# Kernel tuning notes

Measured on AMD Instinct MI355X. Metric: run time of the kernel, lower is better.

Reference implementation:

```python
import jax, jax.numpy as jnp
import numpy as np

PZ = 16          # partition_size
ITERS = 3        # soft_skel iterations
ADP_SMOOTH = 1e-08
A = 0.5
B = 0.5
THRESHOLD = 0.8


def _blockify(x, pz):
    # x: (N, C, Z, X, Y) -> (N*nz*nx*ny, C, pz, pz, pz), loop order N,z,x,y
    N, C, Z, X, Y = x.shape
    nz, nx, ny = Z // pz, X // pz, Y // pz
    x = x.reshape(N, C, nz, pz, nx, pz, ny, pz)
    x = x.transpose(0, 2, 4, 6, 1, 3, 5, 7)
    return x.reshape(N * nz * nx * ny, C, pz, pz, pz)


def _maxpool3d(x, win, pad):
    # torch max_pool pads with -inf
    return jax.lax.reduce_window(
        x, -jnp.inf, jax.lax.max,
        (1, 1) + win, (1, 1, 1, 1, 1),
        ((0, 0), (0, 0), (pad[0], pad[0]), (pad[1], pad[1]), (pad[2], pad[2])))


def _minpool3d(x, win, pad):
    # -maxpool(-x) == minpool with +inf padding
    return jax.lax.reduce_window(
        x, jnp.inf, jax.lax.min,
        (1, 1) + win, (1, 1, 1, 1, 1),
        ((0, 0), (0, 0), (pad[0], pad[0]), (pad[1], pad[1]), (pad[2], pad[2])))


def _soft_erode(img):
    p1 = _minpool3d(img, (3, 1, 1), (1, 0, 0))
    p2 = _minpool3d(img, (1, 3, 1), (0, 1, 0))
    p3 = _minpool3d(img, (1, 1, 3), (0, 0, 1))
    return jnp.minimum(jnp.minimum(p1, p2), p3)


def _soft_dilate(img):
    return _maxpool3d(img, (3, 3, 3), (1, 1, 1))


def _soft_skel(img, iters):
    img1 = _soft_dilate(_soft_erode(img))
    skel = jax.nn.relu(img - img1)
    for _ in range(iters):
        img = _soft_erode(img)
        img1 = _soft_dilate(_soft_erode(img))
        delta = jax.nn.relu(img - img1)
        skel = skel + jax.nn.relu(delta - skel * delta)
    return skel


def _laplacian_bdr(x):
    # 3x3x3 kernel: all -1 with center 26; per-block conv, zero padding 1
    k = -jnp.ones((27,), dtype=x.dtype).at[13].set(26.0).reshape(1, 1, 3, 3, 3)
    b = jax.lax.conv_general_dilated(
        x, k, window_strides=(1, 1, 1), padding=[(1, 1)] * 3,
        dimension_numbers=('NCDHW', 'OIDHW', 'NCDHW'))
    # clamp(min=0) then threshold at 0.1 -> binary map (zero gradient, as in torch)
    return (b > 0.1).astype(x.dtype)


def _per_channel_dice(p, g, eps=1e-6):
    C = p.shape[1]
    pf = jnp.moveaxis(p, 1, 0).reshape(C, -1)
    gf = jnp.moveaxis(g, 1, 0).reshape(C, -1)
    intersect = jnp.sum(pf * gf, axis=-1)
    denom = jnp.sum(pf * pf, axis=-1) + jnp.sum(gf * gf, axis=-1)
    return 2.0 * intersect / jnp.maximum(denom, eps)


def _tversky_terms(p_blk, g_blk):
    # blocks: (M, C, pz, pz, pz) -> per-block adaptive Tversky loss sum
    M = p_blk.shape[0]
    pf = p_blk.reshape(M, -1)
    gf = g_blk.reshape(M, -1)
    tp = jnp.sum(gf * pf, axis=1)
    fn = jnp.sum(gf * (1.0 - pf), axis=1)
    fp = jnp.sum((1.0 - gf) * pf, axis=1)
    alpha = A + B * ((fp + ADP_SMOOTH) / (fp + fn + ADP_SMOOTH))
    beta = A + B * ((fn + ADP_SMOOTH) / (fp + fn + ADP_SMOOTH))
    return jnp.sum(1.0 - (tp + ADP_SMOOTH) / (tp + alpha * fp + beta * fn + ADP_SMOOTH))


def _forward(pred, groundtruth, w1, w2):
    dice_coeff = jnp.mean(_per_channel_dice(pred, groundtruth))
    dice_loss = 1.0 - jnp.mean(_per_channel_dice(pred, groundtruth))

    p_blk = _blockify(pred, PZ)          # (M, 1, pz, pz, pz)
    g_blk = _blockify(groundtruth, PZ)
    M = p_blk.shape[0]

    pre_bdr = _laplacian_bdr(p_blk)
    gt_bdr = _laplacian_bdr(g_blk)
    pre_cl = _soft_skel(p_blk, ITERS)
    gt_cl = _soft_skel(g_blk, ITERS)

    loss_bdr = _tversky_terms(pre_bdr, gt_bdr)
    loss_cl = _tversky_terms(pre_cl, gt_cl)

    w1s, w2s = w1[0], w2[0]
    edge_loss = (w1s ** -2 * loss_bdr + w2s ** -2 * loss_cl) / (2.0 * M) \
        + jnp.log(1.0 + jnp.abs(w1s) * jnp.abs(w2s))

    return jnp.where(dice_coeff < THRESHOLD, dice_loss, dice_loss + edge_loss)


def setup_inputs() -> dict:
    key = jax.random.key(0)
    k1, k2 = jax.random.split(key)
    shape = (2, 1, 192, 192, 192)
    gt = (jax.random.uniform(k1, shape, dtype=jnp.float32) > 0.7).astype(jnp.float32)
    # pred close to gt so dice_coeff > threshold and the adaptive branch runs
    pred = jnp.clip(gt * 0.9 + 0.05 + 0.02 * jax.random.normal(k2, shape, dtype=jnp.float32), 0.0, 1.0)
    return {
        'pred': pred,
        'groundtruth': gt,
        'w1': jnp.ones((1,), dtype=jnp.float32),
        'w2': jnp.ones((1,), dtype=jnp.float32),
    }


def reference(pred, groundtruth, w1, w2):
    return _forward(pred, groundtruth, w1, w2)
```

## Files before the change

### kernel.cpp

```cpp
#include <hip/hip_runtime.h>
#include <cmath>

#define NBLK 3456

#define DPP_SHR1 0x111
#define DPP_SHL1 0x101

template<int CTRL>
__device__ __forceinline__ float dpp_keep_f(float v) {
  return __int_as_float(__builtin_amdgcn_update_dpp(
      __float_as_int(v), __float_as_int(v), CTRL, 0xF, 0xF, false));
}
template<int CTRL>
__device__ __forceinline__ float dpp_zero_f(float v) {
  return __int_as_float(__builtin_amdgcn_update_dpp(
      0, __float_as_int(v), CTRL, 0xF, 0xF, true));
}
template<int CTRL>
__device__ __forceinline__ unsigned dpp_keep_u(unsigned v) {
  return (unsigned)__builtin_amdgcn_update_dpp((int)v, (int)v, CTRL, 0xF, 0xF, false);
}
template<int CTRL>
__device__ __forceinline__ unsigned dpp_zero_u(unsigned v) {
  return (unsigned)__builtin_amdgcn_update_dpp(0, (int)v, CTRL, 0xF, 0xF, true);
}

#define COL_IDX(c, xx) (((c)*18 + (xx) + 1)*16 + y)

__global__ __launch_bounds__(256)
void fused_blocks(const float* __restrict__ pred, const float* __restrict__ gtp,
                  float* __restrict__ ws)
{
  __shared__ float4 buf[1152];
  unsigned* m_ex = (unsigned*)buf;
  float*    red  = ((float*)buf) + 512;

  const int tid = threadIdx.x;
  const int x = tid >> 4;
  const int y = tid & 15;

  const int b  = blockIdx.x;
  const int n  = b / 1728;
  const int r  = b - n * 1728;
  const int bz = r / 144;
  const int r2 = r - bz * 144;
  const int bx = r2 / 12;
  const int by = r2 - bx * 12;

  const size_t base = (size_t)(n * 192 + bz * 16) * 36864
                    + (size_t)(bx * 16 + x) * 192 + (size_t)(by * 16 + y);

  const float INF = __builtin_inff();

  auto write_pads = [&](float pv) {
    if (tid < 128) {
      const int c  = tid >> 5;
      const int xi = ((tid >> 4) & 1) ? 17 : 0;
      const int yy = tid & 15;
      buf[(c * 18 + xi) * 16 + yy] = make_float4(pv, pv, pv, pv);
    }
  };

  float p[16];
  #pragma unroll
  for (int z = 0; z < 16; ++z) p[z] = pred[base + (size_t)z * 36864];

  unsigned gm = 0u;
  float sp2 = 0.f, spg = 0.f;
  #pragma unroll
  for (int z = 0; z < 16; ++z) {
    float gz = gtp[base + (size_t)z * 36864];
    sp2 = fmaf(p[z], p[z], sp2);
    spg = fmaf(p[z], gz, spg);
    if (gz > 0.5f) gm |= (1u << z);
  }

  float szy[16];
  {
    float sy[16];
    #pragma unroll
    for (int z = 0; z < 16; ++z) {
      float v = p[z];
      sy[z] = v + dpp_zero_f<DPP_SHR1>(v) + dpp_zero_f<DPP_SHL1>(v);
    }
    #pragma unroll
    for (int z = 0; z < 16; ++z) {
      float s = sy[z];
      if (z > 0)  s += sy[z-1];
      if (z < 15) s += sy[z+1];
      szy[z] = s;
    }
  }
  #pragma unroll
  for (int c = 0; c < 4; ++c)
    buf[COL_IDX(c, x)] = make_float4(szy[4*c], szy[4*c+1], szy[4*c+2], szy[4*c+3]);
  write_pads(0.f);
  __syncthreads();

  unsigned pm_bdr = 0u;
  #pragma unroll
  for (int c = 0; c < 4; ++c) {
    float4 a4 = buf[COL_IDX(c, x - 1)];
    float4 b4 = buf[COL_IDX(c, x + 1)];
    float sm[4] = {a4.x + b4.x, a4.y + b4.y, a4.z + b4.z, a4.w + b4.w};
    #pragma unroll
    for (int j = 0; j < 4; ++j) {
      const int z = 4*c + j;
      float bb = fmaf(27.f, p[z], -(szy[z] + sm[j]));
      if (bb > 0.1f) pm_bdr |= (1u << z);
    }
  }
  __syncthreads();

  #pragma unroll
  for (int c = 0; c < 4; ++c)
    buf[COL_IDX(c, x)] = make_float4(p[4*c], p[4*c+1], p[4*c+2], p[4*c+3]);
  write_pads(INF);
  __syncthreads();

  float cur[16], skl[16];
  #pragma unroll
  for (int z = 0; z < 16; ++z) { cur[z] = p[z]; skl[z] = 0.f; }

  for (int k = 0; k < 4; ++k) {
    float xm[16], xp[16];
    #pragma unroll
    for (int c = 0; c < 4; ++c) {
      float4 a4 = buf[COL_IDX(c, x - 1)];
      float4 b4 = buf[COL_IDX(c, x + 1)];
      xm[4*c] = a4.x; xm[4*c+1] = a4.y; xm[4*c+2] = a4.z; xm[4*c+3] = a4.w;
      xp[4*c] = b4.x; xp[4*c+1] = b4.y; xp[4*c+2] = b4.z; xp[4*c+3] = b4.w;
    }
    float en[16];
    #pragma unroll
    for (int z = 0; z < 16; ++z) {
      float v = cur[z];
      float m = fminf(v, fminf(dpp_keep_f<DPP_SHR1>(v), dpp_keep_f<DPP_SHL1>(v)));
      if (z > 0)  m = fminf(m, cur[z-1]);
      if (z < 15) m = fminf(m, cur[z+1]);
      en[z] = fminf(m, fminf(xm[z], xp[z]));
    }
    float ty[16], tz[16];
    #pragma unroll
    for (int z = 0; z < 16; ++z) {
      float v = en[z];
      ty[z] = fmaxf(v, fmaxf(dpp_keep_f<DPP_SHR1>(v), dpp_keep_f<DPP_SHL1>(v)));
    }
    #pragma unroll
    for (int z = 0; z < 16; ++z) {
      float m = ty[z];
      if (z > 0)  m = fmaxf(m, ty[z-1]);
      if (z < 15) m = fmaxf(m, ty[z+1]);
      tz[z] = m;
    }
    __syncthreads();
    #pragma unroll
    for (int c = 0; c < 4; ++c)
      buf[COL_IDX(c, x)] = make_float4(tz[4*c], tz[4*c+1], tz[4*c+2], tz[4*c+3]);
    write_pads(-INF);
    __syncthreads();
    #pragma unroll
    for (int c = 0; c < 4; ++c) {
      float4 a4 = buf[COL_IDX(c, x - 1)];
      float4 b4 = buf[COL_IDX(c, x + 1)];
      float dm[4] = {fmaxf(a4.x, b4.x), fmaxf(a4.y, b4.y),
                     fmaxf(a4.z, b4.z), fmaxf(a4.w, b4.w)};
      #pragma unroll
      for (int j = 0; j < 4; ++j) {
        const int z = 4*c + j;
        float D = fmaxf(tz[z], dm[j]);
        float delta = fmaxf(cur[z] - D, 0.f);
        skl[z] += fmaxf(fmaf(-skl[z], delta, delta), 0.f);
        cur[z] = en[z];
      }
    }
    if (k < 3) {
      __syncthreads();
      #pragma unroll
      for (int c = 0; c < 4; ++c)
        buf[COL_IDX(c, x)] = make_float4(en[4*c], en[4*c+1], en[4*c+2], en[4*c+3]);
      write_pads(INF);
      __syncthreads();
    }
  }
  __syncthreads();

  unsigned ly  = gm & dpp_zero_u<DPP_SHR1>(gm) & dpp_zero_u<DPP_SHL1>(gm);
  unsigned lzy = ly & (ly >> 1) & ((ly << 1) & 0xFFFFu);
  m_ex[(x + 1) * 16 + y] = lzy;
  if (tid < 32) m_ex[((tid >> 4) ? 17 : 0) * 16 + (tid & 15)] = 0u;
  __syncthreads();
  unsigned gm_bdr = gm & ~(m_ex[x * 16 + y] & lzy & m_ex[(x + 2) * 16 + y]);

  unsigned curm = gm, sklm = 0u;
  for (int k = 0; k < 4; ++k) {
    __syncthreads();
    m_ex[(x + 1) * 16 + y] = curm;
    if (tid < 32) m_ex[((tid >> 4) ? 17 : 0) * 16 + (tid & 15)] = 0xFFFFu;
    __syncthreads();
    unsigned em = curm
        & dpp_keep_u<DPP_SHR1>(curm) & dpp_keep_u<DPP_SHL1>(curm)
        & ((curm >> 1) | 0x8000u) & ((curm << 1) | 1u)
        & m_ex[x * 16 + y] & m_ex[(x + 2) * 16 + y];
    em &= 0xFFFFu;
    unsigned dy  = em | dpp_keep_u<DPP_SHR1>(em) | dpp_keep_u<DPP_SHL1>(em);
    unsigned dzy = (dy | (dy >> 1) | (dy << 1)) & 0xFFFFu;
    __syncthreads();
    m_ex[(x + 1) * 16 + y] = dzy;
    if (tid < 32) m_ex[((tid >> 4) ? 17 : 0) * 16 + (tid & 15)] = 0u;
    __syncthreads();
    unsigned D = m_ex[x * 16 + y] | dzy | m_ex[(x + 2) * 16 + y];
    sklm |= curm & ~D;
    curm = em;
  }

  float vals[9];
  {
    float tcl = 0.f, scl = 0.f;
    #pragma unroll
    for (int z = 0; z < 16; ++z) {
      scl += skl[z];
      tcl += ((sklm >> z) & 1u) ? skl[z] : 0.f;
    }
    vals[0] = tcl;
    vals[1] = scl;
    vals[2] = (float)__popc(sklm);
    vals[3] = (float)__popc(pm_bdr & gm_bdr);
    vals[4] = (float)__popc(pm_bdr);
    vals[5] = (float)__popc(gm_bdr);
    vals[6] = spg;
    vals[7] = sp2;
    vals[8] = (float)__popc(gm);
  }
  #pragma unroll
  for (int j = 0; j < 9; ++j) {
    float v = vals[j];
    #pragma unroll
    for (int off = 32; off; off >>= 1) v += __shfl_xor(v, off);
    vals[j] = v;
  }
  if ((tid & 63) == 0) {
    #pragma unroll
    for (int j = 0; j < 9; ++j) red[(tid >> 6) * 9 + j] = vals[j];
  }
  __syncthreads();
  if (tid == 0) {
    float t[9];
    #pragma unroll
    for (int j = 0; j < 9; ++j) t[j] = red[j] + red[9 + j] + red[18 + j] + red[27 + j];
    const float s = 1e-8f;
    float tp = t[3], fp = t[4] - t[3], fn = t[5] - t[3];
    float den = fp + fn + s;
    float alpha = 0.5f + 0.5f * ((fp + s) / den);
    float beta  = 0.5f + 0.5f * ((fn + s) / den);
    float lb = 1.f - (tp + s) / (tp + alpha * fp + beta * fn + s);
    float tpc = t[0], fpc = t[1] - t[0], fnc = t[2] - t[0];
    float denc = fpc + fnc + s;
    float alphac = 0.5f + 0.5f * ((fpc + s) / denc);
    float betac  = 0.5f + 0.5f * ((fnc + s) / denc);
    float lc = 1.f - (tpc + s) / (tpc + alphac * fpc + betac * fnc + s);
    float* o = ws + (size_t)b * 8;
    o[0] = lb; o[1] = lc; o[2] = t[6]; o[3] = t[7]; o[4] = t[8];
  }
}

__global__ __launch_bounds__(256)
void finalize_kernel(const float* __restrict__ ws, const float* __restrict__ w1p,
                     const float* __restrict__ w2p, float* __restrict__ out)
{
  __shared__ double red2[20];
  double a[5] = {0.0, 0.0, 0.0, 0.0, 0.0};
  for (int i = threadIdx.x; i < NBLK; i += 256) {
    const float* o = ws + (size_t)i * 8;
    a[0] += (double)o[0];
    a[1] += (double)o[1];
    a[2] += (double)o[2];
    a[3] += (double)o[3];
    a[4] += (double)o[4];
  }
  #pragma unroll
  for (int j = 0; j < 5; ++j) {
    double v = a[j];
    #pragma unroll
    for (int off = 32; off; off >>= 1) v += __shfl_xor(v, off);
    if ((threadIdx.x & 63) == 0) red2[(threadIdx.x >> 6) * 5 + j] = v;
  }
  __syncthreads();
  if (threadIdx.x == 0) {
    double t[5];
    #pragma unroll
    for (int j = 0; j < 5; ++j) t[j] = red2[j] + red2[5 + j] + red2[10 + j] + red2[15 + j];
    double denom = t[3] + t[4];
    if (denom < 1e-6) denom = 1e-6;
    double dice = 2.0 * t[2] / denom;
    double dl = 1.0 - dice;
    double w1 = (double)w1p[0], w2 = (double)w2p[0];
    double edge = (t[0] / (w1 * w1) + t[1] / (w2 * w2)) / (2.0 * (double)NBLK)
                + log(1.0 + fabs(w1) * fabs(w2));
    out[0] = (float)((dice < 0.8) ? dl : (dl + edge));
  }
}

extern "C" void kernel_launch(void* const* d_in, const int* in_sizes, int n_in,
                              void* d_out, int out_size, void* d_ws, size_t ws_size,
                              hipStream_t stream)
{
  const float* pred = (const float*)d_in[0];
  const float* gtp  = (const float*)d_in[1];
  const float* w1   = (const float*)d_in[2];
  const float* w2   = (const float*)d_in[3];
  float* ws = (float*)d_ws;

  fused_blocks<<<NBLK, 256, 0, stream>>>(pred, gtp, ws);
  finalize_kernel<<<1, 256, 0, stream>>>(ws, w1, w2, (float*)d_out);
}
```

Baseline: 181.0 us.

## Split each block's z-column across two threads and double-buffer shared memory

Each 16^3 block is now processed by 512 threads, with two threads per (x,y) column each owning 8 z-slices. Z-boundary neighbours are exchanged with cross-lane shuffles. Separate erode and dilate shared buffers, plus two bitmask buffers, remove several barriers per iteration and let the tz stencil be folded into the shared read. This targets per-thread register pressure and serial latency, at the cost of extra shuffles, larger shared memory per block and redundant bitmask work in the duplicated half.

```diff
diff --git a/kernel.cpp b/kernel.cpp
--- a/kernel.cpp
+++ b/kernel.cpp
@@ -25,19 +25,22 @@
   return (unsigned)__builtin_amdgcn_update_dpp(0, (int)v, CTRL, 0xF, 0xF, true);
 }
 
-#define COL_IDX(c, xx) (((c)*18 + (xx) + 1)*16 + y)
-
-__global__ __launch_bounds__(256)
+#define COL_IDX(cg, xx) (((cg)*18 + (xx) + 1)*16 + y)
+
+__global__ __launch_bounds__(512)
 void fused_blocks(const float* __restrict__ pred, const float* __restrict__ gtp,
                   float* __restrict__ ws)
 {
-  __shared__ float4 buf[1152];
-  unsigned* m_ex = (unsigned*)buf;
-  float*    red  = ((float*)buf) + 512;
+  __shared__ float4   bufE[1152];
+  __shared__ float4   bufT[1152];
+  __shared__ unsigned mA[288];
+  __shared__ unsigned mB[288];
+  float* red = (float*)mB;
 
   const int tid = threadIdx.x;
-  const int x = tid >> 4;
-  const int y = tid & 15;
+  const int y  = tid & 15;
+  const int zh = (tid >> 4) & 1;
+  const int x  = tid >> 5;
 
   const int b  = blockIdx.x;
   const int n  = b / 1728;
@@ -47,190 +50,193 @@
   const int bx = r2 / 12;
   const int by = r2 - bx * 12;
 
-  const size_t base = (size_t)(n * 192 + bz * 16) * 36864
+  const size_t base = (size_t)(n * 192 + bz * 16 + zh * 8) * 36864
                     + (size_t)(bx * 16 + x) * 192 + (size_t)(by * 16 + y);
 
   const float INF = __builtin_inff();
-
-  auto write_pads = [&](float pv) {
+  const int cg0 = zh * 2, cg1 = zh * 2 + 1;
+
+  auto write_padsE = [&](float pv) {
     if (tid < 128) {
-      const int c  = tid >> 5;
+      const int cg = tid >> 5;
       const int xi = ((tid >> 4) & 1) ? 17 : 0;
-      const int yy = tid & 15;
-      buf[(c * 18 + xi) * 16 + yy] = make_float4(pv, pv, pv, pv);
+      bufE[(cg * 18 + xi) * 16 + (tid & 15)] = make_float4(pv, pv, pv, pv);
     }
   };
-
-  float p[16];
-  #pragma unroll
-  for (int z = 0; z < 16; ++z) p[z] = pred[base + (size_t)z * 36864];
-
-  unsigned gm = 0u;
+  auto write_padsT = [&](float pv) {
+    if (tid >= 128 && tid < 256) {
+      const int t = tid - 128;
+      const int cg = t >> 5;
+      const int xi = ((t >> 4) & 1) ? 17 : 0;
+      bufT[(cg * 18 + xi) * 16 + (t & 15)] = make_float4(pv, pv, pv, pv);
+    }
+  };
+
+  float p[8];
+  #pragma unroll
+  for (int j = 0; j < 8; ++j) p[j] = pred[base + (size_t)j * 36864];
+
+  unsigned own8 = 0u;
   float sp2 = 0.f, spg = 0.f;
   #pragma unroll
-  for (int z = 0; z < 16; ++z) {
-    float gz = gtp[base + (size_t)z * 36864];
-    sp2 = fmaf(p[z], p[z], sp2);
-    spg = fmaf(p[z], gz, spg);
-    if (gz > 0.5f) gm |= (1u << z);
-  }
-
-  float szy[16];
+  for (int j = 0; j < 8; ++j) {
+    float gz = gtp[base + (size_t)j * 36864];
+    sp2 = fmaf(p[j], p[j], sp2);
+    spg = fmaf(p[j], gz, spg);
+    if (gz > 0.5f) own8 |= (1u << j);
+  }
+  unsigned gsh = own8 << (zh * 8);
+  unsigned gmfull = gsh | (unsigned)__shfl_xor((int)gsh, 16);
+
+  float szy[8];
   {
-    float sy[16];
-    #pragma unroll
-    for (int z = 0; z < 16; ++z) {
-      float v = p[z];
-      sy[z] = v + dpp_zero_f<DPP_SHR1>(v) + dpp_zero_f<DPP_SHL1>(v);
-    }
-    #pragma unroll
-    for (int z = 0; z < 16; ++z) {
-      float s = sy[z];
-      if (z > 0)  s += sy[z-1];
-      if (z < 15) s += sy[z+1];
-      szy[z] = s;
-    }
-  }
-  #pragma unroll
-  for (int c = 0; c < 4; ++c)
-    buf[COL_IDX(c, x)] = make_float4(szy[4*c], szy[4*c+1], szy[4*c+2], szy[4*c+3]);
-  write_pads(0.f);
+    float sy[8];
+    #pragma unroll
+    for (int j = 0; j < 8; ++j) {
+      float v = p[j];
+      sy[j] = v + dpp_zero_f<DPP_SHR1>(v) + dpp_zero_f<DPP_SHL1>(v);
+    }
+    float bsy = __shfl_xor(zh ? sy[0] : sy[7], 16);
+    #pragma unroll
+    for (int j = 0; j < 8; ++j) {
+      float prev = (j > 0) ? sy[j-1] : (zh ? bsy : 0.f);
+      float next = (j < 7) ? sy[j+1] : (zh ? 0.f : bsy);
+      szy[j] = prev + sy[j] + next;
+    }
+  }
+  bufT[COL_IDX(cg0, x)] = make_float4(szy[0], szy[1], szy[2], szy[3]);
+  bufT[COL_IDX(cg1, x)] = make_float4(szy[4], szy[5], szy[6], szy[7]);
+  write_padsT(0.f);
+  bufE[COL_IDX(cg0, x)] = make_float4(p[0], p[1], p[2], p[3]);
+  bufE[COL_IDX(cg1, x)] = make_float4(p[4], p[5], p[6], p[7]);
+  write_padsE(INF);
   __syncthreads();
 
-  unsigned pm_bdr = 0u;
-  #pragma unroll
-  for (int c = 0; c < 4; ++c) {
-    float4 a4 = buf[COL_IDX(c, x - 1)];
-    float4 b4 = buf[COL_IDX(c, x + 1)];
-    float sm[4] = {a4.x + b4.x, a4.y + b4.y, a4.z + b4.z, a4.w + b4.w};
-    #pragma unroll
-    for (int j = 0; j < 4; ++j) {
-      const int z = 4*c + j;
-      float bb = fmaf(27.f, p[z], -(szy[z] + sm[j]));
-      if (bb > 0.1f) pm_bdr |= (1u << z);
-    }
-  }
+  unsigned pm8 = 0u;
+  #pragma unroll
+  for (int c = 0; c < 2; ++c) {
+    float4 a4 = bufT[COL_IDX(cg0 + c, x - 1)];
+    float4 b4 = bufT[COL_IDX(cg0 + c, x + 1)];
+    #pragma unroll
+    for (int jj = 0; jj < 4; ++jj) {
+      const int j = 4*c + jj;
+      float bb = fmaf(27.f, p[j], -(szy[j] + ((&a4.x)[jj] + (&b4.x)[jj])));
+      if (bb > 0.1f) pm8 |= (1u << j);
+    }
+  }
+
+  float cur[8], skl[8];
+  #pragma unroll
+  for (int j = 0; j < 8; ++j) { cur[j] = p[j]; skl[j] = 0.f; }
+
+  for (int k = 0; k < 4; ++k) {
+    float en[8];
+    float bcur = __shfl_xor(zh ? cur[0] : cur[7], 16);
+    #pragma unroll
+    for (int c = 0; c < 2; ++c) {
+      float4 a4 = bufE[COL_IDX(cg0 + c, x - 1)];
+      float4 b4 = bufE[COL_IDX(cg0 + c, x + 1)];
+      #pragma unroll
+      for (int jj = 0; jj < 4; ++jj) {
+        const int j = 4*c + jj;
+        float v  = cur[j];
+        float m1 = fminf(dpp_keep_f<DPP_SHR1>(v), v);
+        float m2 = fminf(dpp_keep_f<DPP_SHL1>(v), m1);
+        float zl = (j > 0) ? cur[j-1] : (zh ? bcur : v);
+        float zu = (j < 7) ? cur[j+1] : (zh ? v : bcur);
+        en[j] = fminf(fminf(m2, fminf(zl, zu)),
+                      fminf((&a4.x)[jj], (&b4.x)[jj]));
+      }
+    }
+    __syncthreads();
+
+    bufE[COL_IDX(cg0, x)] = make_float4(en[0], en[1], en[2], en[3]);
+    bufE[COL_IDX(cg1, x)] = make_float4(en[4], en[5], en[6], en[7]);
+    write_padsE(INF);
+    float ty[8];
+    #pragma unroll
+    for (int j = 0; j < 8; ++j) {
+      float v = en[j];
+      ty[j] = fmaxf(fmaxf(dpp_keep_f<DPP_SHR1>(v), dpp_keep_f<DPP_SHL1>(v)), v);
+    }
+    float bty = __shfl_xor(zh ? ty[0] : ty[7], 16);
+    #pragma unroll
+    for (int c = 0; c < 2; ++c) {
+      float4 w;
+      #pragma unroll
+      for (int jj = 0; jj < 4; ++jj) {
+        const int j = 4*c + jj;
+        float prev = (j > 0) ? ty[j-1] : (zh ? bty : -INF);
+        float next = (j < 7) ? ty[j+1] : (zh ? -INF : bty);
+        (&w.x)[jj] = fmaxf(fmaxf(prev, ty[j]), next);
+      }
+      bufT[COL_IDX(cg0 + c, x)] = w;
+    }
+    write_padsT(-INF);
+    __syncthreads();
+
+    #pragma unroll
+    for (int c = 0; c < 2; ++c) {
+      float4 a4 = bufT[COL_IDX(cg0 + c, x - 1)];
+      float4 b4 = bufT[COL_IDX(cg0 + c, x + 1)];
+      float4 c4 = bufT[COL_IDX(cg0 + c, x)];
+      #pragma unroll
+      for (int jj = 0; jj < 4; ++jj) {
+        const int j = 4*c + jj;
+        float D = fmaxf(fmaxf((&a4.x)[jj], (&b4.x)[jj]), (&c4.x)[jj]);
+        float delta = fmaxf(cur[j] - D, 0.f);
+        skl[j] += fmaxf(fmaf(-skl[j], delta, delta), 0.f);
+        cur[j] = en[j];
+      }
+    }
+  }
+
+  unsigned ly  = gmfull & dpp_zero_u<DPP_SHR1>(gmfull) & dpp_zero_u<DPP_SHL1>(gmfull);
+  unsigned lzy = ly & (ly >> 1) & ((ly << 1) & 0xFFFFu);
+  if (!zh) mA[(x + 1) * 16 + y] = lzy;
+  if (tid < 32) mA[((tid >> 4) ? 17 : 0) * 16 + (tid & 15)] = 0u;
   __syncthreads();
-
-  #pragma unroll
-  for (int c = 0; c < 4; ++c)
-    buf[COL_IDX(c, x)] = make_float4(p[4*c], p[4*c+1], p[4*c+2], p[4*c+3]);
-  write_pads(INF);
-  __syncthreads();
-
-  float cur[16], skl[16];
-  #pragma unroll
-  for (int z = 0; z < 16; ++z) { cur[z] = p[z]; skl[z] = 0.f; }
-
+  unsigned gm_bdr = gmfull & ~(mA[x * 16 + y] & lzy & mA[(x + 2) * 16 + y]);
+
+  unsigned curm = gmfull, sklm = 0u;
   for (int k = 0; k < 4; ++k) {
-    float xm[16], xp[16];
-    #pragma unroll
-    for (int c = 0; c < 4; ++c) {
-      float4 a4 = buf[COL_IDX(c, x - 1)];
-      float4 b4 = buf[COL_IDX(c, x + 1)];
-      xm[4*c] = a4.x; xm[4*c+1] = a4.y; xm[4*c+2] = a4.z; xm[4*c+3] = a4.w;
-      xp[4*c] = b4.x; xp[4*c+1] = b4.y; xp[4*c+2] = b4.z; xp[4*c+3] = b4.w;
-    }
-    float en[16];
-    #pragma unroll
-    for (int z = 0; z < 16; ++z) {
-      float v = cur[z];
-      float m = fminf(v, fminf(dpp_keep_f<DPP_SHR1>(v), dpp_keep_f<DPP_SHL1>(v)));
-      if (z > 0)  m = fminf(m, cur[z-1]);
-      if (z < 15) m = fminf(m, cur[z+1]);
-      en[z] = fminf(m, fminf(xm[z], xp[z]));
-    }
-    float ty[16], tz[16];
-    #pragma unroll
-    for (int z = 0; z < 16; ++z) {
-      float v = en[z];
-      ty[z] = fmaxf(v, fmaxf(dpp_keep_f<DPP_SHR1>(v), dpp_keep_f<DPP_SHL1>(v)));
-    }
-    #pragma unroll
-    for (int z = 0; z < 16; ++z) {
-      float m = ty[z];
-      if (z > 0)  m = fmaxf(m, ty[z-1]);
-      if (z < 15) m = fmaxf(m, ty[z+1]);
-      tz[z] = m;
-    }
-    __syncthreads();
-    #pragma unroll
-    for (int c = 0; c < 4; ++c)
-      buf[COL_IDX(c, x)] = make_float4(tz[4*c], tz[4*c+1], tz[4*c+2], tz[4*c+3]);
-    write_pads(-INF);
-    __syncthreads();
-    #pragma unroll
-    for (int c = 0; c < 4; ++c) {
-      float4 a4 = buf[COL_IDX(c, x - 1)];
-      float4 b4 = buf[COL_IDX(c, x + 1)];
-      float dm[4] = {fmaxf(a4.x, b4.x), fmaxf(a4.y, b4.y),
-                     fmaxf(a4.z, b4.z), fmaxf(a4.w, b4.w)};
-      #pragma unroll
-      for (int j = 0; j < 4; ++j) {
-        const int z = 4*c + j;
-        float D = fmaxf(tz[z], dm[j]);
-        float delta = fmaxf(cur[z] - D, 0.f);
-        skl[z] += fmaxf(fmaf(-skl[z], delta, delta), 0.f);
-        cur[z] = en[z];
-      }
-    }
-    if (k < 3) {
-      __syncthreads();
-      #pragma unroll
-      for (int c = 0; c < 4; ++c)
-        buf[COL_IDX(c, x)] = make_float4(en[4*c], en[4*c+1], en[4*c+2], en[4*c+3]);
-      write_pads(INF);
-      __syncthreads();
-    }
-  }
-  __syncthreads();
-
-  unsigned ly  = gm & dpp_zero_u<DPP_SHR1>(gm) & dpp_zero_u<DPP_SHL1>(gm);
-  unsigned lzy = ly & (ly >> 1) & ((ly << 1) & 0xFFFFu);
-  m_ex[(x + 1) * 16 + y] = lzy;
-  if (tid < 32) m_ex[((tid >> 4) ? 17 : 0) * 16 + (tid & 15)] = 0u;
-  __syncthreads();
-  unsigned gm_bdr = gm & ~(m_ex[x * 16 + y] & lzy & m_ex[(x + 2) * 16 + y]);
-
-  unsigned curm = gm, sklm = 0u;
-  for (int k = 0; k < 4; ++k) {
-    __syncthreads();
-    m_ex[(x + 1) * 16 + y] = curm;
-    if (tid < 32) m_ex[((tid >> 4) ? 17 : 0) * 16 + (tid & 15)] = 0xFFFFu;
+    if (!zh) mB[(x + 1) * 16 + y] = curm;
+    if (tid < 32) mB[((tid >> 4) ? 17 : 0) * 16 + (tid & 15)] = 0xFFFFu;
     __syncthreads();
     unsigned em = curm
         & dpp_keep_u<DPP_SHR1>(curm) & dpp_keep_u<DPP_SHL1>(curm)
         & ((curm >> 1) | 0x8000u) & ((curm << 1) | 1u)
-        & m_ex[x * 16 + y] & m_ex[(x + 2) * 16 + y];
+        & mB[x * 16 + y] & mB[(x + 2) * 16 + y];
     em &= 0xFFFFu;
     unsigned dy  = em | dpp_keep_u<DPP_SHR1>(em) | dpp_keep_u<DPP_SHL1>(em);
     unsigned dzy = (dy | (dy >> 1) | (dy << 1)) & 0xFFFFu;
+    if (!zh) mA[(x + 1) * 16 + y] = dzy;
+    if (tid < 32) mA[((tid >> 4) ? 17 : 0) * 16 + (tid & 15)] = 0u;
     __syncthreads();
-    m_ex[(x + 1) * 16 + y] = dzy;
-    if (tid < 32) m_ex[((tid >> 4) ? 17 : 0) * 16 + (tid & 15)] = 0u;
-    __syncthreads();
-    unsigned D = m_ex[x * 16 + y] | dzy | m_ex[(x + 2) * 16 + y];
+    unsigned D = mA[x * 16 + y] | dzy | mA[(x + 2) * 16 + y];
     sklm |= curm & ~D;
     curm = em;
   }
 
   float vals[9];
   {
+    unsigned sklm8  = (sklm   >> (zh * 8)) & 0xFFu;
+    unsigned gmbdr8 = (gm_bdr >> (zh * 8)) & 0xFFu;
     float tcl = 0.f, scl = 0.f;
     #pragma unroll
-    for (int z = 0; z < 16; ++z) {
-      scl += skl[z];
-      tcl += ((sklm >> z) & 1u) ? skl[z] : 0.f;
+    for (int j = 0; j < 8; ++j) {
+      scl += skl[j];
+      tcl += ((sklm8 >> j) & 1u) ? skl[j] : 0.f;
     }
     vals[0] = tcl;
     vals[1] = scl;
-    vals[2] = (float)__popc(sklm);
-    vals[3] = (float)__popc(pm_bdr & gm_bdr);
-    vals[4] = (float)__popc(pm_bdr);
-    vals[5] = (float)__popc(gm_bdr);
+    vals[2] = (float)__popc(sklm8);
+    vals[3] = (float)__popc(pm8 & gmbdr8);
+    vals[4] = (float)__popc(pm8);
+    vals[5] = (float)__popc(gmbdr8);
     vals[6] = spg;
     vals[7] = sp2;
-    vals[8] = (float)__popc(gm);
+    vals[8] = (float)__popc(own8);
   }
   #pragma unroll
   for (int j = 0; j < 9; ++j) {
@@ -247,7 +253,12 @@
   if (tid == 0) {
     float t[9];
     #pragma unroll
-    for (int j = 0; j < 9; ++j) t[j] = red[j] + red[9 + j] + red[18 + j] + red[27 + j];
+    for (int j = 0; j < 9; ++j) {
+      float s4 = 0.f;
+      #pragma unroll
+      for (int w = 0; w < 8; ++w) s4 += red[w * 9 + j];
+      t[j] = s4;
+    }
     const float s = 1e-8f;
     float tp = t[3], fp = t[4] - t[3], fn = t[5] - t[3];
     float den = fp + fn + s;
@@ -311,6 +322,6 @@
   const float* w2   = (const float*)d_in[3];
   float* ws = (float*)d_ws;
 
-  fused_blocks<<<NBLK, 256, 0, stream>>>(pred, gtp, ws);
+  fused_blocks<<<NBLK, 512, 0, stream>>>(pred, gtp, ws);
   finalize_kernel<<<1, 256, 0, stream>>>(ws, w1, w2, (float*)d_out);
 }
```

Measured after the change: 197.2 us. +9.0%, slower.
